# Kernel optimization log

Measured on AMD Instinct MI355X. Metric: run time of the kernel, lower is better.

The kernel has to match this reference:

```python
import jax, jax.numpy as jnp
import numpy as np

D_EMBED = 1024
D_CROSS = 768
N_HEADS = 16
D_HEAD = D_EMBED // N_HEADS


def setup_inputs() -> dict:
    key = jax.random.key(0)
    ks = jax.random.split(key, 10)
    s = 0.02
    return {
        "x": jax.random.normal(ks[0], (4, 4096, D_EMBED), dtype=jnp.float32),
        "y": jax.random.normal(ks[1], (4, 1024, D_CROSS), dtype=jnp.float32),
        "Wq": jax.random.normal(ks[2], (D_EMBED, D_EMBED), dtype=jnp.float32) * s,
        "bq": jnp.zeros((D_EMBED,), dtype=jnp.float32),
        "Wk": jax.random.normal(ks[3], (D_CROSS, D_EMBED), dtype=jnp.float32) * s,
        "bk": jnp.zeros((D_EMBED,), dtype=jnp.float32),
        "Wv": jax.random.normal(ks[4], (D_CROSS, D_EMBED), dtype=jnp.float32) * s,
        "bv": jnp.zeros((D_EMBED,), dtype=jnp.float32),
        "Wo": jax.random.normal(ks[5], (D_EMBED, D_EMBED), dtype=jnp.float32) * s,
        "bo": jnp.zeros((D_EMBED,), dtype=jnp.float32),
    }


def reference(x, y, Wq, bq, Wk, bk, Wv, bv, Wo, bo):
    b, sq, _ = x.shape
    skv = y.shape[1]
    # projections
    q = x @ Wq + bq   # [b, sq, d_embed]
    k = y @ Wk + bk   # [b, skv, d_embed]
    v = y @ Wv + bv   # [b, skv, d_embed]
    # split heads: [b, h, s, d_head]
    q = q.reshape(b, sq, N_HEADS, D_HEAD).transpose(0, 2, 1, 3)
    k = k.reshape(b, skv, N_HEADS, D_HEAD).transpose(0, 2, 1, 3)
    v = v.reshape(b, skv, N_HEADS, D_HEAD).transpose(0, 2, 1, 3)
    scale = 1.0 / jnp.sqrt(jnp.float32(D_HEAD))
    scores = jnp.einsum("bhqd,bhkd->bhqk", q, k) * scale
    attn = jax.nn.softmax(scores, axis=-1)
    out = jnp.einsum("bhqk,bhkd->bhqd", attn, v)
    out = out.transpose(0, 2, 1, 3).reshape(b, sq, D_EMBED)
    return out @ Wo + bo
```

## Files before the change

kernel.cpp:

```cpp
#include <hip/hip_runtime.h>

typedef unsigned short ushort_t;
typedef __attribute__((ext_vector_type(8))) __bf16 bf16x8;
typedef __attribute__((ext_vector_type(4))) float floatx4;
typedef __attribute__((ext_vector_type(8))) unsigned short ushortx8;
typedef __attribute__((ext_vector_type(4))) unsigned short ushortx4;
typedef __attribute__((ext_vector_type(4))) short short4v;
typedef __attribute__((ext_vector_type(2))) unsigned uint2v;

__device__ __forceinline__ ushort_t f2bf(float f) {
    union { float f; unsigned u; } v; v.f = f;
    unsigned r = v.u + 0x7fffu + ((v.u >> 16) & 1u);
    return (ushort_t)(r >> 16);
}

__device__ __forceinline__ void gld_lds16(const ushort_t* g, ushort_t* l) {
    __builtin_amdgcn_global_load_lds(
        (const __attribute__((address_space(1))) unsigned*)g,
        (__attribute__((address_space(3))) unsigned*)l, 16, 0, 0);
}

__device__ __forceinline__ unsigned pk_bf16(float a, float b) {
    unsigned ua = __builtin_bit_cast(unsigned, a) + 0x8000u;
    unsigned ub = __builtin_bit_cast(unsigned, b) + 0x8000u;
    return __builtin_amdgcn_perm(ub, ua, 0x07060302u);
}

__global__ void cvt_all(const float* __restrict__ x, const float* __restrict__ y,
                        ushort_t* __restrict__ xb, ushort_t* __restrict__ yb) {
    const int NX = 4194304;
    int i = blockIdx.x * 256 + threadIdx.x;
    float4 v; ushortx4* dst;
    if (i < NX) { v = ((const float4*)x)[i]; dst = (ushortx4*)xb + i; }
    else        { int j = i - NX; v = ((const float4*)y)[j]; dst = (ushortx4*)yb + j; }
    ushortx4 o;
    o.x = f2bf(v.x); o.y = f2bf(v.y); o.z = f2bf(v.z); o.w = f2bf(v.w);
    *dst = o;
}

__global__ void transpose_cvt2(const float* __restrict__ W0, const float* __restrict__ W1,
                               ushort_t* __restrict__ D0, ushort_t* __restrict__ D1,
                               int K, int N) {
    const float* W = blockIdx.z ? W1 : W0;
    ushort_t* Wt = blockIdx.z ? D1 : D0;
    __shared__ ushort_t t[32][33];
    const int n0 = blockIdx.x * 32, k0 = blockIdx.y * 32;
    const int tx = threadIdx.x & 31, ty = threadIdx.x >> 5;
#pragma unroll
    for (int i = 0; i < 4; ++i)
        t[ty + 8 * i][tx] = f2bf(W[(size_t)(k0 + ty + 8 * i) * N + n0 + tx]);
    __syncthreads();
#pragma unroll
    for (int i = 0; i < 4; ++i)
        Wt[(size_t)(n0 + ty + 8 * i) * K + k0 + tx] = t[tx][ty + 8 * i];
}

template <int MODE>
__global__ __launch_bounds__(256) void gemm_bt_bias(
    const ushort_t* __restrict__ A, const ushort_t* __restrict__ Bt,
    const float* __restrict__ bias, void* __restrict__ Cv,
    int M, int N, int K, float scale) {
    __shared__ __align__(16) ushort_t As[128 * 32];
    __shared__ __align__(16) ushort_t Bs[128 * 32];
    const int tid = threadIdx.x;
    const int lane = tid & 63, w = tid >> 6;
    const int quad = lane >> 4, l16 = lane & 15;
    const int wr = w >> 1, wc = w & 1;
    const int m0 = blockIdx.x * 128, n0 = blockIdx.y * 128;

    floatx4 acc[4][4] = {};

    const ushort_t* ga0 = A + (size_t)(m0 + (tid >> 2)) * K + (tid & 3) * 8;
    const ushort_t* ga1 = A + (size_t)(m0 + 64 + (tid >> 2)) * K + (tid & 3) * 8;
    const ushort_t* gb0 = Bt + (size_t)(n0 + (tid >> 2)) * K + (tid & 3) * 8;
    const ushort_t* gb1 = Bt + (size_t)(n0 + 64 + (tid >> 2)) * K + (tid & 3) * 8;
    ushort_t* la0 = As + tid * 8;
    ushort_t* la1 = As + (tid + 256) * 8;
    ushort_t* lb0 = Bs + tid * 8;
    ushort_t* lb1 = Bs + (tid + 256) * 8;

    for (int kt = 0; kt < K; kt += 32) {
        __syncthreads();
        gld_lds16(ga0, la0); gld_lds16(ga1, la1);
        gld_lds16(gb0, lb0); gld_lds16(gb1, lb1);
        ga0 += 32; ga1 += 32; gb0 += 32; gb1 += 32;
        __syncthreads();
        bf16x8 af[4], bfr[4];
#pragma unroll
        for (int i = 0; i < 4; ++i)
            af[i] = *(const bf16x8*)(As + (wr * 64 + i * 16 + l16) * 32 + quad * 8);
#pragma unroll
        for (int j = 0; j < 4; ++j)
            bfr[j] = *(const bf16x8*)(Bs + (wc * 64 + j * 16 + l16) * 32 + quad * 8);
#pragma unroll
        for (int i = 0; i < 4; ++i)
#pragma unroll
            for (int j = 0; j < 4; ++j)
                acc[i][j] = __builtin_amdgcn_mfma_f32_16x16x32_bf16(af[i], bfr[j], acc[i][j], 0, 0, 0);
    }

#pragma unroll
    for (int i = 0; i < 4; ++i) {
        const int rowb = m0 + wr * 64 + i * 16 + quad * 4;
#pragma unroll
        for (int j = 0; j < 4; ++j) {
            const int col = n0 + wc * 64 + j * 16 + l16;
            const float bv = bias[col];
            if (MODE == 0) {
#pragma unroll
                for (int r = 0; r < 4; ++r)
                    ((float*)Cv)[(size_t)(rowb + r) * N + col] = (acc[i][j][r] + bv) * scale;
            } else {
                const int h = col >> 6, d = col & 63;
                const int bq_ = rowb >> 12, q = rowb & 4095;
                ushort_t* base = (ushort_t*)Cv +
                    (((size_t)bq_ * 16 + h) * 32 + (q >> 7)) * 8192 +
                    (d >> 3) * 1024 + (size_t)(q & 127) * 8 + (d & 7);
#pragma unroll
                for (int r = 0; r < 4; ++r)
                    base[r * 8] = f2bf((acc[i][j][r] + bv) * scale);
            }
        }
    }
}

__global__ __launch_bounds__(256) void gemm_kv(
    const ushort_t* __restrict__ A, const ushort_t* __restrict__ Bt,
    const float* __restrict__ bk, const float* __restrict__ bv,
    ushort_t* __restrict__ Kc, ushort_t* __restrict__ Vc) {
    const int K = 768;
    __shared__ __align__(16) ushort_t As[128 * 32];
    __shared__ __align__(16) ushort_t Bs[128 * 32];
    const int tid = threadIdx.x;
    const int lane = tid & 63, w = tid >> 6;
    const int quad = lane >> 4, l16 = lane & 15;
    const int wr = w >> 1, wc = w & 1;
    const int m0 = blockIdx.x * 128, n0 = blockIdx.y * 128;

    floatx4 acc[4][4] = {};

    const ushort_t* ga0 = A + (size_t)(m0 + (tid >> 2)) * K + (tid & 3) * 8;
    const ushort_t* ga1 = A + (size_t)(m0 + 64 + (tid >> 2)) * K + (tid & 3) * 8;
    const ushort_t* gb0 = Bt + (size_t)(n0 + (tid >> 2)) * K + (tid & 3) * 8;
    const ushort_t* gb1 = Bt + (size_t)(n0 + 64 + (tid >> 2)) * K + (tid & 3) * 8;
    ushort_t* la0 = As + tid * 8;
    ushort_t* la1 = As + (tid + 256) * 8;
    ushort_t* lb0 = Bs + tid * 8;
    ushort_t* lb1 = Bs + (tid + 256) * 8;

    for (int kt = 0; kt < K; kt += 32) {
        __syncthreads();
        gld_lds16(ga0, la0); gld_lds16(ga1, la1);
        gld_lds16(gb0, lb0); gld_lds16(gb1, lb1);
        ga0 += 32; ga1 += 32; gb0 += 32; gb1 += 32;
        __syncthreads();
        bf16x8 af[4], bfr[4];
#pragma unroll
        for (int i = 0; i < 4; ++i)
            af[i] = *(const bf16x8*)(As + (wr * 64 + i * 16 + l16) * 32 + quad * 8);
#pragma unroll
        for (int j = 0; j < 4; ++j)
            bfr[j] = *(const bf16x8*)(Bs + (wc * 64 + j * 16 + l16) * 32 + quad * 8);
#pragma unroll
        for (int i = 0; i < 4; ++i)
#pragma unroll
            for (int j = 0; j < 4; ++j)
                acc[i][j] = __builtin_amdgcn_mfma_f32_16x16x32_bf16(af[i], bfr[j], acc[i][j], 0, 0, 0);
    }

    if (n0 < 1024) {
#pragma unroll
        for (int i = 0; i < 4; ++i) {
            const int rowb = m0 + wr * 64 + i * 16 + quad * 4;
            const int b = rowb >> 10, kvt = (rowb & 1023) >> 6, kvr = rowb & 63;
#pragma unroll
            for (int j = 0; j < 4; ++j) {
                const int col = n0 + wc * 64 + j * 16 + l16;
                const int h = col >> 6, d = col & 63;
                const float bval = bk[col];
                ushort_t* base = Kc + (((size_t)b * 16 + h) * 16 + kvt) * 4096 +
                                 (d >> 3) * 512 + kvr * 8 + (d & 7);
#pragma unroll
                for (int r = 0; r < 4; ++r)
                    base[r * 8] = f2bf(acc[i][j][r] + bval);
            }
        }
    } else {
#pragma unroll
        for (int i = 0; i < 4; ++i) {
            const int rowb = m0 + wr * 64 + i * 16 + quad * 4;
            const int b = rowb >> 10, kvt = (rowb & 1023) >> 6, sub = (rowb >> 3) & 7;
#pragma unroll
            for (int j = 0; j < 4; ++j) {
                const int col = n0 + wc * 64 + j * 16 + l16;
                const int nc = col - 1024;
                const int h = nc >> 6, d = nc & 63;
                const float bval = bv[nc];
                ushortx4 o;
#pragma unroll
                for (int r = 0; r < 4; ++r) o[r] = f2bf(acc[i][j][r] + bval);
                *(ushortx4*)(Vc + (((size_t)b * 16 + h) * 16 + kvt) * 4096 +
                             sub * 512 + d * 8 + (quad & 1) * 4) = o;
            }
        }
    }
}

__device__ __forceinline__ void stage_kv(const ushort_t* kg, const ushort_t* vg,
                                         ushort_t* dst, int tid) {
#pragma unroll
    for (int i = 0; i < 2; ++i) {
        int s = i * 256 + tid;
        gld_lds16(kg + s * 8, dst + s * 8);
        gld_lds16(vg + s * 8, dst + 4096 + s * 8);
    }
}

__global__ __launch_bounds__(256) void attn_kernel(
    const ushort_t* __restrict__ Qc,
    const ushort_t* __restrict__ Kc,
    const ushort_t* __restrict__ Vc,
    ushort_t* __restrict__ O)
{
    __shared__ __align__(16) ushort_t smem[24576];
    ushort_t* Qs = smem;
    const int tid = threadIdx.x;
    const int w = tid >> 6, lane = tid & 63;
    const int quad = lane >> 4, l16 = lane & 15;
    const int q0 = blockIdx.x * 128;
    const int bh = blockIdx.y, b = bh >> 4;

    const ushort_t* qg = Qc + ((size_t)bh * 32 + blockIdx.x) * 8192;
#pragma unroll
    for (int i = 0; i < 4; ++i) {
        int s = i * 256 + tid;
        gld_lds16(qg + s * 8, Qs + s * 8);
    }
    const ushort_t* kvbase = Kc + (size_t)bh * 65536;
    const ushort_t* vvbase = Vc + (size_t)bh * 65536;
    stage_kv(kvbase, vvbase, smem + 8192, tid);
    __syncthreads();

    floatx4 oacc[4][2] = {};
    float lsum[2] = {0.f, 0.f};

    for (int kvt = 0; kvt < 16; ++kvt) {
        const int sel = kvt & 1;
        if (kvt < 15)
            stage_kv(kvbase + (kvt + 1) * 4096, vvbase + (kvt + 1) * 4096,
                     smem + 8192 + (sel ^ 1) * 8192, tid);
        const ushort_t* pK = smem + 8192 + sel * 8192;
        const ushort_t* pV = pK + 4096;

        floatx4 st[4][2] = {};
#pragma unroll
        for (int ks = 0; ks < 2; ++ks) {
            bf16x8 ak[4], bq[2];
#pragma unroll
            for (int m4 = 0; m4 < 4; ++m4)
                ak[m4] = *(const bf16x8*)(pK + ((ks * 4 + quad) * 64 + m4 * 16 + l16) * 8);
#pragma unroll
            for (int qt = 0; qt < 2; ++qt)
                bq[qt] = *(const bf16x8*)(Qs + ((ks * 4 + quad) * 128 + w * 32 + qt * 16 + l16) * 8);
#pragma unroll
            for (int m4 = 0; m4 < 4; ++m4)
#pragma unroll
                for (int qt = 0; qt < 2; ++qt)
                    st[m4][qt] = __builtin_amdgcn_mfma_f32_16x16x32_bf16(ak[m4], bq[qt], st[m4][qt], 0, 0, 0);
        }

        uint2v pk[4][2];
#pragma unroll
        for (int qt = 0; qt < 2; ++qt) {
            float acc = 0.f;
#pragma unroll
            for (int m4 = 0; m4 < 4; ++m4) {
                float p0 = __builtin_amdgcn_exp2f(st[m4][qt][0]);
                float p1 = __builtin_amdgcn_exp2f(st[m4][qt][1]);
                float p2 = __builtin_amdgcn_exp2f(st[m4][qt][2]);
                float p3 = __builtin_amdgcn_exp2f(st[m4][qt][3]);
                acc += (p0 + p1) + (p2 + p3);
                pk[m4][qt].x = pk_bf16(p0, p1);
                pk[m4][qt].y = pk_bf16(p2, p3);
            }
            lsum[qt] += acc;
        }

#pragma unroll
        for (int m4 = 0; m4 < 4; ++m4) {
#pragma unroll
            for (int dt = 0; dt < 4; ++dt) {
                short4v av = *(const short4v*)(pV +
                    ((m4 * 2 + (quad >> 1)) * 64 + dt * 16 + l16) * 8 + (quad & 1) * 4);
#pragma unroll
                for (int qt = 0; qt < 2; ++qt) {
                    short4v bp = __builtin_bit_cast(short4v, pk[m4][qt]);
                    oacc[dt][qt] = __builtin_amdgcn_mfma_f32_16x16x16bf16_1k(av, bp, oacc[dt][qt], 0, 0, 0);
                }
            }
        }
        __syncthreads();
    }

    const int h = bh & 15;
    float inv[2];
#pragma unroll
    for (int qt = 0; qt < 2; ++qt) {
        float l = lsum[qt];
        l += __shfl_xor(l, 16, 64);
        l += __shfl_xor(l, 32, 64);
        inv[qt] = 1.0f / l;
    }
#pragma unroll
    for (int dt = 0; dt < 4; ++dt)
#pragma unroll
        for (int qt = 0; qt < 2; ++qt) {
            uint2v o2;
            o2.x = pk_bf16(oacc[dt][qt][0] * inv[qt], oacc[dt][qt][1] * inv[qt]);
            o2.y = pk_bf16(oacc[dt][qt][2] * inv[qt], oacc[dt][qt][3] * inv[qt]);
            *(uint2v*)(smem + (w * 32 + qt * 16 + l16) * 68 + dt * 16 + quad * 4) = o2;
        }
    __syncthreads();
#pragma unroll
    for (int i = 0; i < 8; ++i) {
        int s = i * 256 + tid;
        int row = s >> 4, dc = s & 15;
        ushortx4 v = *(const ushortx4*)(smem + row * 68 + dc * 4);
        *(ushortx4*)(O + (size_t)(b * 4096 + q0 + row) * 1024 + h * 64 + dc * 4) = v;
    }
}

extern "C" void kernel_launch(void* const* d_in, const int* in_sizes, int n_in,
                              void* d_out, int out_size, void* d_ws, size_t ws_size,
                              hipStream_t stream) {
    const float* x  = (const float*)d_in[0];
    const float* y  = (const float*)d_in[1];
    const float* Wq = (const float*)d_in[2];
    const float* bq = (const float*)d_in[3];
    const float* Wk = (const float*)d_in[4];
    const float* bk = (const float*)d_in[5];
    const float* Wv = (const float*)d_in[6];
    const float* bv = (const float*)d_in[7];
    const float* Wo = (const float*)d_in[8];
    const float* bo = (const float*)d_in[9];

    char* ws = (char*)d_ws;
    ushort_t* xb   = (ushort_t*)(ws);
    ushort_t* yb   = (ushort_t*)(ws + 33554432);
    ushort_t* Wqt  = (ushort_t*)(ws + 39845888);
    ushort_t* Wkvt = (ushort_t*)(ws + 41943040);
    ushort_t* Wot  = (ushort_t*)(ws + 45088768);
    ushort_t* Qc   = (ushort_t*)(ws + 47185920);
    ushort_t* Kc   = (ushort_t*)(ws + 80740352);
    ushort_t* Vc   = (ushort_t*)(ws + 89128960);
    ushort_t* Ab   = (ushort_t*)(ws + 97517568);

    const float QSCALE = 0.125f * 1.44269504f;

    cvt_all<<<19456, 256, 0, stream>>>(x, y, xb, yb);
    transpose_cvt2<<<dim3(32, 32, 2), 256, 0, stream>>>(Wq, Wo, Wqt, Wot, 1024, 1024);
    transpose_cvt2<<<dim3(32, 24, 2), 256, 0, stream>>>(Wk, Wv, Wkvt, Wkvt + 786432, 768, 1024);

    gemm_bt_bias<1><<<dim3(128, 8), 256, 0, stream>>>(xb, Wqt, bq, Qc, 16384, 1024, 1024, QSCALE);
    gemm_kv<<<dim3(32, 16), 256, 0, stream>>>(yb, Wkvt, bk, bv, Kc, Vc);

    attn_kernel<<<dim3(32, 64), 256, 0, stream>>>(Qc, Kc, Vc, Ab);

    gemm_bt_bias<0><<<dim3(128, 8), 256, 0, stream>>>(Ab, Wot, bo, (float*)d_out, 16384, 1024, 1024, 1.0f);
}
```

Measured before the change: 395.4 us.

## Merge prep and projection launches; keep Q fragments in registers in attention

Folds the input-conversion and weight-transpose kernels into one launch, and the Q and KV projection GEMMs into a single grid, cutting launches from seven to four and letting the smaller KV GEMM fill spare CUs. The attention kernel now loads its Q fragments straight from global memory into registers instead of staging them through LDS. This shrinks shared memory from 48KB to 32KB and adds a launch-bounds occupancy hint. The cost is extra registers for the Q fragments, which may cause spills under the occupancy hint.

```diff
diff --git a/kernel.cpp b/kernel.cpp
--- a/kernel.cpp
+++ b/kernel.cpp
@@ -26,50 +26,56 @@
     return __builtin_amdgcn_perm(ub, ua, 0x07060302u);
 }
 
-__global__ void cvt_all(const float* __restrict__ x, const float* __restrict__ y,
-                        ushort_t* __restrict__ xb, ushort_t* __restrict__ yb) {
-    const int NX = 4194304;
-    int i = blockIdx.x * 256 + threadIdx.x;
-    float4 v; ushortx4* dst;
-    if (i < NX) { v = ((const float4*)x)[i]; dst = (ushortx4*)xb + i; }
-    else        { int j = i - NX; v = ((const float4*)y)[j]; dst = (ushortx4*)yb + j; }
-    ushortx4 o;
-    o.x = f2bf(v.x); o.y = f2bf(v.y); o.z = f2bf(v.z); o.w = f2bf(v.w);
-    *dst = o;
-}
-
-__global__ void transpose_cvt2(const float* __restrict__ W0, const float* __restrict__ W1,
-                               ushort_t* __restrict__ D0, ushort_t* __restrict__ D1,
-                               int K, int N) {
-    const float* W = blockIdx.z ? W1 : W0;
-    ushort_t* Wt = blockIdx.z ? D1 : D0;
+__global__ __launch_bounds__(256) void prep(
+    const float* __restrict__ x, const float* __restrict__ y,
+    const float* __restrict__ Wq, const float* __restrict__ Wo,
+    const float* __restrict__ Wk, const float* __restrict__ Wv,
+    ushort_t* __restrict__ xb, ushort_t* __restrict__ yb,
+    ushort_t* __restrict__ Wqt, ushort_t* __restrict__ Wot,
+    ushort_t* __restrict__ Wkvt) {
+    const int bid = blockIdx.x;
+    if (bid < 19456) {
+        const int NX = 4194304;
+        int i = bid * 256 + threadIdx.x;
+        float4 v; ushortx4* dst;
+        if (i < NX) { v = ((const float4*)x)[i]; dst = (ushortx4*)xb + i; }
+        else        { int j = i - NX; v = ((const float4*)y)[j]; dst = (ushortx4*)yb + j; }
+        ushortx4 o;
+        o.x = f2bf(v.x); o.y = f2bf(v.y); o.z = f2bf(v.z); o.w = f2bf(v.w);
+        *dst = o;
+        return;
+    }
     __shared__ ushort_t t[32][33];
-    const int n0 = blockIdx.x * 32, k0 = blockIdx.y * 32;
+    const float* W; ushort_t* Wt; int K, n0, k0;
+    if (bid < 21504) {
+        int tt = bid - 19456;
+        W = (tt >> 10) ? Wo : Wq;
+        Wt = (tt >> 10) ? Wot : Wqt;
+        K = 1024;
+        int r = tt & 1023;
+        n0 = (r & 31) * 32; k0 = (r >> 5) * 32;
+    } else {
+        int tt = bid - 21504;
+        int z = tt / 768, r = tt - z * 768;
+        W = z ? Wv : Wk;
+        Wt = Wkvt + (size_t)z * 786432;
+        K = 768;
+        n0 = (r & 31) * 32; k0 = (r >> 5) * 32;
+    }
     const int tx = threadIdx.x & 31, ty = threadIdx.x >> 5;
 #pragma unroll
     for (int i = 0; i < 4; ++i)
-        t[ty + 8 * i][tx] = f2bf(W[(size_t)(k0 + ty + 8 * i) * N + n0 + tx]);
+        t[ty + 8 * i][tx] = f2bf(W[(size_t)(k0 + ty + 8 * i) * 1024 + n0 + tx]);
     __syncthreads();
 #pragma unroll
     for (int i = 0; i < 4; ++i)
         Wt[(size_t)(n0 + ty + 8 * i) * K + k0 + tx] = t[tx][ty + 8 * i];
 }
 
-template <int MODE>
-__global__ __launch_bounds__(256) void gemm_bt_bias(
+__device__ __forceinline__ void gemm_core(
     const ushort_t* __restrict__ A, const ushort_t* __restrict__ Bt,
-    const float* __restrict__ bias, void* __restrict__ Cv,
-    int M, int N, int K, float scale) {
-    __shared__ __align__(16) ushort_t As[128 * 32];
-    __shared__ __align__(16) ushort_t Bs[128 * 32];
-    const int tid = threadIdx.x;
-    const int lane = tid & 63, w = tid >> 6;
-    const int quad = lane >> 4, l16 = lane & 15;
-    const int wr = w >> 1, wc = w & 1;
-    const int m0 = blockIdx.x * 128, n0 = blockIdx.y * 128;
-
-    floatx4 acc[4][4] = {};
-
+    int K, int m0, int n0, ushort_t* As, ushort_t* Bs,
+    floatx4 (&acc)[4][4], int tid, int wr, int wc, int quad, int l16) {
     const ushort_t* ga0 = A + (size_t)(m0 + (tid >> 2)) * K + (tid & 3) * 8;
     const ushort_t* ga1 = A + (size_t)(m0 + 64 + (tid >> 2)) * K + (tid & 3) * 8;
     const ushort_t* gb0 = Bt + (size_t)(n0 + (tid >> 2)) * K + (tid & 3) * 8;
@@ -98,37 +104,89 @@
             for (int j = 0; j < 4; ++j)
                 acc[i][j] = __builtin_amdgcn_mfma_f32_16x16x32_bf16(af[i], bfr[j], acc[i][j], 0, 0, 0);
     }
-
-#pragma unroll
-    for (int i = 0; i < 4; ++i) {
-        const int rowb = m0 + wr * 64 + i * 16 + quad * 4;
-#pragma unroll
-        for (int j = 0; j < 4; ++j) {
-            const int col = n0 + wc * 64 + j * 16 + l16;
-            const float bv = bias[col];
-            if (MODE == 0) {
+}
+
+__global__ __launch_bounds__(256) void proj(
+    const ushort_t* __restrict__ xb, const ushort_t* __restrict__ yb,
+    const ushort_t* __restrict__ Wqt, const ushort_t* __restrict__ Wkvt,
+    const float* __restrict__ bq, const float* __restrict__ bk, const float* __restrict__ bv,
+    ushort_t* __restrict__ Qc, ushort_t* __restrict__ Kc, ushort_t* __restrict__ Vc,
+    float qscale) {
+    __shared__ __align__(16) ushort_t As[128 * 32];
+    __shared__ __align__(16) ushort_t Bs[128 * 32];
+    const int tid = threadIdx.x;
+    const int lane = tid & 63, w = tid >> 6;
+    const int quad = lane >> 4, l16 = lane & 15;
+    const int wr = w >> 1, wc = w & 1;
+    const int id = blockIdx.x;
+    floatx4 acc[4][4] = {};
+
+    if (id < 1024) {
+        const int m0 = (id >> 3) * 128, n0 = (id & 7) * 128;
+        gemm_core(xb, Wqt, 1024, m0, n0, As, Bs, acc, tid, wr, wc, quad, l16);
+#pragma unroll
+        for (int i = 0; i < 4; ++i) {
+            const int rowb = m0 + wr * 64 + i * 16 + quad * 4;
+#pragma unroll
+            for (int j = 0; j < 4; ++j) {
+                const int col = n0 + wc * 64 + j * 16 + l16;
+                const float bval = bq[col];
+                const int h = col >> 6, d = col & 63;
+                const int b_ = rowb >> 12, q = rowb & 4095;
+                ushort_t* base = Qc +
+                    (((size_t)b_ * 16 + h) * 32 + (q >> 7)) * 8192 +
+                    (d >> 3) * 1024 + (size_t)(q & 127) * 8 + (d & 7);
 #pragma unroll
                 for (int r = 0; r < 4; ++r)
-                    ((float*)Cv)[(size_t)(rowb + r) * N + col] = (acc[i][j][r] + bv) * scale;
-            } else {
-                const int h = col >> 6, d = col & 63;
-                const int bq_ = rowb >> 12, q = rowb & 4095;
-                ushort_t* base = (ushort_t*)Cv +
-                    (((size_t)bq_ * 16 + h) * 32 + (q >> 7)) * 8192 +
-                    (d >> 3) * 1024 + (size_t)(q & 127) * 8 + (d & 7);
-#pragma unroll
-                for (int r = 0; r < 4; ++r)
-                    base[r * 8] = f2bf((acc[i][j][r] + bv) * scale);
-            }
-        }
-    }
-}
-
-__global__ __launch_bounds__(256) void gemm_kv(
+                    base[r * 8] = f2bf((acc[i][j][r] + bval) * qscale);
+            }
+        }
+    } else {
+        const int id2 = id - 1024;
+        const int m0 = (id2 & 31) * 128, n0 = (id2 >> 5) * 128;
+        gemm_core(yb, Wkvt, 768, m0, n0, As, Bs, acc, tid, wr, wc, quad, l16);
+        if (n0 < 1024) {
+#pragma unroll
+            for (int i = 0; i < 4; ++i) {
+                const int rowb = m0 + wr * 64 + i * 16 + quad * 4;
+                const int b = rowb >> 10, kvt = (rowb & 1023) >> 6, kvr = rowb & 63;
+#pragma unroll
+                for (int j = 0; j < 4; ++j) {
+                    const int col = n0 + wc * 64 + j * 16 + l16;
+                    const int h = col >> 6, d = col & 63;
+                    const float bval = bk[col];
+                    ushort_t* base = Kc + (((size_t)b * 16 + h) * 16 + kvt) * 4096 +
+                                     (d >> 3) * 512 + kvr * 8 + (d & 7);
+#pragma unroll
+                    for (int r = 0; r < 4; ++r)
+                        base[r * 8] = f2bf(acc[i][j][r] + bval);
+                }
+            }
+        } else {
+#pragma unroll
+            for (int i = 0; i < 4; ++i) {
+                const int rowb = m0 + wr * 64 + i * 16 + quad * 4;
+                const int b = rowb >> 10, kvt = (rowb & 1023) >> 6, sub = (rowb >> 3) & 7;
+#pragma unroll
+                for (int j = 0; j < 4; ++j) {
+                    const int col = n0 + wc * 64 + j * 16 + l16;
+                    const int nc = col - 1024;
+                    const int h = nc >> 6, d = nc & 63;
+                    const float bval = bv[nc];
+                    ushortx4 o;
+#pragma unroll
+                    for (int r = 0; r < 4; ++r) o[r] = f2bf(acc[i][j][r] + bval);
+                    *(ushortx4*)(Vc + (((size_t)b * 16 + h) * 16 + kvt) * 4096 +
+                                 sub * 512 + d * 8 + (quad & 1) * 4) = o;
+                }
+            }
+        }
+    }
+}
+
+__global__ __launch_bounds__(256) void gemm_o(
     const ushort_t* __restrict__ A, const ushort_t* __restrict__ Bt,
-    const float* __restrict__ bk, const float* __restrict__ bv,
-    ushort_t* __restrict__ Kc, ushort_t* __restrict__ Vc) {
-    const int K = 768;
+    const float* __restrict__ bias, float* __restrict__ C, int N, int K) {
     __shared__ __align__(16) ushort_t As[128 * 32];
     __shared__ __align__(16) ushort_t Bs[128 * 32];
     const int tid = threadIdx.x;
@@ -136,72 +194,18 @@
     const int quad = lane >> 4, l16 = lane & 15;
     const int wr = w >> 1, wc = w & 1;
     const int m0 = blockIdx.x * 128, n0 = blockIdx.y * 128;
-
     floatx4 acc[4][4] = {};
-
-    const ushort_t* ga0 = A + (size_t)(m0 + (tid >> 2)) * K + (tid & 3) * 8;
-    const ushort_t* ga1 = A + (size_t)(m0 + 64 + (tid >> 2)) * K + (tid & 3) * 8;
-    const ushort_t* gb0 = Bt + (size_t)(n0 + (tid >> 2)) * K + (tid & 3) * 8;
-    const ushort_t* gb1 = Bt + (size_t)(n0 + 64 + (tid >> 2)) * K + (tid & 3) * 8;
-    ushort_t* la0 = As + tid * 8;
-    ushort_t* la1 = As + (tid + 256) * 8;
-    ushort_t* lb0 = Bs + tid * 8;
-    ushort_t* lb1 = Bs + (tid + 256) * 8;
-
-    for (int kt = 0; kt < K; kt += 32) {
-        __syncthreads();
-        gld_lds16(ga0, la0); gld_lds16(ga1, la1);
-        gld_lds16(gb0, lb0); gld_lds16(gb1, lb1);
-        ga0 += 32; ga1 += 32; gb0 += 32; gb1 += 32;
-        __syncthreads();
-        bf16x8 af[4], bfr[4];
-#pragma unroll
-        for (int i = 0; i < 4; ++i)
-            af[i] = *(const bf16x8*)(As + (wr * 64 + i * 16 + l16) * 32 + quad * 8);
-#pragma unroll
-        for (int j = 0; j < 4; ++j)
-            bfr[j] = *(const bf16x8*)(Bs + (wc * 64 + j * 16 + l16) * 32 + quad * 8);
-#pragma unroll
-        for (int i = 0; i < 4; ++i)
-#pragma unroll
-            for (int j = 0; j < 4; ++j)
-                acc[i][j] = __builtin_amdgcn_mfma_f32_16x16x32_bf16(af[i], bfr[j], acc[i][j], 0, 0, 0);
-    }
-
-    if (n0 < 1024) {
-#pragma unroll
-        for (int i = 0; i < 4; ++i) {
-            const int rowb = m0 + wr * 64 + i * 16 + quad * 4;
-            const int b = rowb >> 10, kvt = (rowb & 1023) >> 6, kvr = rowb & 63;
-#pragma unroll
-            for (int j = 0; j < 4; ++j) {
-                const int col = n0 + wc * 64 + j * 16 + l16;
-                const int h = col >> 6, d = col & 63;
-                const float bval = bk[col];
-                ushort_t* base = Kc + (((size_t)b * 16 + h) * 16 + kvt) * 4096 +
-                                 (d >> 3) * 512 + kvr * 8 + (d & 7);
-#pragma unroll
-                for (int r = 0; r < 4; ++r)
-                    base[r * 8] = f2bf(acc[i][j][r] + bval);
-            }
-        }
-    } else {
-#pragma unroll
-        for (int i = 0; i < 4; ++i) {
-            const int rowb = m0 + wr * 64 + i * 16 + quad * 4;
-            const int b = rowb >> 10, kvt = (rowb & 1023) >> 6, sub = (rowb >> 3) & 7;
-#pragma unroll
-            for (int j = 0; j < 4; ++j) {
-                const int col = n0 + wc * 64 + j * 16 + l16;
-                const int nc = col - 1024;
-                const int h = nc >> 6, d = nc & 63;
-                const float bval = bv[nc];
-                ushortx4 o;
-#pragma unroll
-                for (int r = 0; r < 4; ++r) o[r] = f2bf(acc[i][j][r] + bval);
-                *(ushortx4*)(Vc + (((size_t)b * 16 + h) * 16 + kvt) * 4096 +
-                             sub * 512 + d * 8 + (quad & 1) * 4) = o;
-            }
+    gemm_core(A, Bt, K, m0, n0, As, Bs, acc, tid, wr, wc, quad, l16);
+#pragma unroll
+    for (int i = 0; i < 4; ++i) {
+        const int rowb = m0 + wr * 64 + i * 16 + quad * 4;
+#pragma unroll
+        for (int j = 0; j < 4; ++j) {
+            const int col = n0 + wc * 64 + j * 16 + l16;
+            const float bval = bias[col];
+#pragma unroll
+            for (int r = 0; r < 4; ++r)
+                C[(size_t)(rowb + r) * N + col] = acc[i][j][r] + bval;
         }
     }
 }
@@ -216,14 +220,13 @@
     }
 }
 
-__global__ __launch_bounds__(256) void attn_kernel(
+__global__ __launch_bounds__(256, 4) void attn_kernel(
     const ushort_t* __restrict__ Qc,
     const ushort_t* __restrict__ Kc,
     const ushort_t* __restrict__ Vc,
     ushort_t* __restrict__ O)
 {
-    __shared__ __align__(16) ushort_t smem[24576];
-    ushort_t* Qs = smem;
+    __shared__ __align__(16) ushort_t smem[16384];
     const int tid = threadIdx.x;
     const int w = tid >> 6, lane = tid & 63;
     const int quad = lane >> 4, l16 = lane & 15;
@@ -231,14 +234,17 @@
     const int bh = blockIdx.y, b = bh >> 4;
 
     const ushort_t* qg = Qc + ((size_t)bh * 32 + blockIdx.x) * 8192;
-#pragma unroll
-    for (int i = 0; i < 4; ++i) {
-        int s = i * 256 + tid;
-        gld_lds16(qg + s * 8, Qs + s * 8);
-    }
+    bf16x8 qf[2][2];
+#pragma unroll
+    for (int ks = 0; ks < 2; ++ks)
+#pragma unroll
+        for (int qt = 0; qt < 2; ++qt)
+            qf[ks][qt] = *(const bf16x8*)(qg +
+                ((ks * 4 + quad) * 128 + w * 32 + qt * 16 + l16) * 8);
+
     const ushort_t* kvbase = Kc + (size_t)bh * 65536;
     const ushort_t* vvbase = Vc + (size_t)bh * 65536;
-    stage_kv(kvbase, vvbase, smem + 8192, tid);
+    stage_kv(kvbase, vvbase, smem, tid);
     __syncthreads();
 
     floatx4 oacc[4][2] = {};
@@ -248,25 +254,22 @@
         const int sel = kvt & 1;
         if (kvt < 15)
             stage_kv(kvbase + (kvt + 1) * 4096, vvbase + (kvt + 1) * 4096,
-                     smem + 8192 + (sel ^ 1) * 8192, tid);
-        const ushort_t* pK = smem + 8192 + sel * 8192;
+                     smem + (sel ^ 1) * 8192, tid);
+        const ushort_t* pK = smem + sel * 8192;
         const ushort_t* pV = pK + 4096;
 
         floatx4 st[4][2] = {};
 #pragma unroll
         for (int ks = 0; ks < 2; ++ks) {
-            bf16x8 ak[4], bq[2];
+            bf16x8 ak[4];
 #pragma unroll
             for (int m4 = 0; m4 < 4; ++m4)
                 ak[m4] = *(const bf16x8*)(pK + ((ks * 4 + quad) * 64 + m4 * 16 + l16) * 8);
 #pragma unroll
-            for (int qt = 0; qt < 2; ++qt)
-                bq[qt] = *(const bf16x8*)(Qs + ((ks * 4 + quad) * 128 + w * 32 + qt * 16 + l16) * 8);
-#pragma unroll
             for (int m4 = 0; m4 < 4; ++m4)
 #pragma unroll
                 for (int qt = 0; qt < 2; ++qt)
-                    st[m4][qt] = __builtin_amdgcn_mfma_f32_16x16x32_bf16(ak[m4], bq[qt], st[m4][qt], 0, 0, 0);
+                    st[m4][qt] = __builtin_amdgcn_mfma_f32_16x16x32_bf16(ak[m4], qf[ks][qt], st[m4][qt], 0, 0, 0);
         }
 
         uint2v pk[4][2];
@@ -357,14 +360,8 @@
 
     const float QSCALE = 0.125f * 1.44269504f;
 
-    cvt_all<<<19456, 256, 0, stream>>>(x, y, xb, yb);
-    transpose_cvt2<<<dim3(32, 32, 2), 256, 0, stream>>>(Wq, Wo, Wqt, Wot, 1024, 1024);
-    transpose_cvt2<<<dim3(32, 24, 2), 256, 0, stream>>>(Wk, Wv, Wkvt, Wkvt + 786432, 768, 1024);
-
-    gemm_bt_bias<1><<<dim3(128, 8), 256, 0, stream>>>(xb, Wqt, bq, Qc, 16384, 1024, 1024, QSCALE);
-    gemm_kv<<<dim3(32, 16), 256, 0, stream>>>(yb, Wkvt, bk, bv, Kc, Vc);
-
+    prep<<<23040, 256, 0, stream>>>(x, y, Wq, Wo, Wk, Wv, xb, yb, Wqt, Wot, Wkvt);
+    proj<<<1536, 256, 0, stream>>>(xb, yb, Wqt, Wkvt, bq, bk, bv, Qc, Kc, Vc, QSCALE);
     attn_kernel<<<dim3(32, 64), 256, 0, stream>>>(Qc, Kc, Vc, Ab);
-
-    gemm_bt_bias<0><<<dim3(128, 8), 256, 0, stream>>>(Ab, Wot, bo, (float*)d_out, 16384, 1024, 1024, 1.0f);
-}
+    gemm_o<<<dim3(128, 8), 256, 0, stream>>>(Ab, Wot, bo, (float*)d_out, 1024, 1024);
+}
```

New measurement: 371.4 us. -6.1%, faster.
